# Kernel optimization log

Measured on AMD Instinct MI355X. Metric: run time of the kernel, lower is better.

## Reference

```python
import jax, jax.numpy as jnp
import numpy as np
from jax import lax

K = 21            # length_p_kernel
PK = K * K        # 441
CENTER = PK // 2  # 220, center of prediction window
EPS = 1e-4
PAD = K // 2


def conv3(x, w, b):
    # 3x3 same-padding conv, NCHW / OIHW
    y = lax.conv_general_dilated(x, w, (1, 1), ((1, 1), (1, 1)),
                                 dimension_numbers=('NCHW', 'OIHW', 'NCHW'))
    return y + b[None, :, None, None]


def unfold(x):
    # torch F.unfold with 21x21 kernel, zero padding 10 -> [b, C, 441, h, w]
    b, c, h, w = x.shape
    p = lax.conv_general_dilated_patches(x, (K, K), (1, 1), ((PAD, PAD), (PAD, PAD)))
    return p.reshape(b, c, PK, h, w)


def setup_inputs() -> dict:
    key = jax.random.key(0)
    ks = jax.random.split(key, 6)
    inp = jax.random.normal(ks[0], (1, 10, 128, 128), dtype=jnp.float32)
    ref = jax.random.normal(ks[1], (1, 3, 128, 128), dtype=jnp.float32)
    w0 = jax.random.normal(ks[2], (100, 10, 3, 3), dtype=jnp.float32) * 0.05
    b0 = jnp.zeros((100,), jnp.float32)
    wmid = jax.random.normal(ks[3], (23, 100, 100, 3, 3), dtype=jnp.float32) * 0.05
    bmid = jnp.zeros((23, 100), jnp.float32)
    wfin = jax.random.normal(ks[4], (441, 100, 3, 3), dtype=jnp.float32) * 0.05
    bfin = jnp.zeros((441,), jnp.float32)
    return {"input": inp, "ref": ref, "w0": w0, "b0": b0,
            "wmid": wmid, "bmid": bmid, "wfin": wfin, "bfin": bfin}


def reference(input, ref, w0, b0, wmid, bmid, wfin, bfin):
    # ref is only used by the (unavailable) loss branch; only_img_out path computed.
    b, _, h, w = input.shape

    x = conv3(input, w0, b0)

    def step(x, wb):
        return jax.nn.leaky_relu(conv3(x, wb[0], wb[1]), 0.01), None
    x, _ = lax.scan(step, x, (wmid, bmid))

    # --- W generator + softmax over 441 kernel-weight channels ---
    W = jax.nn.softmax(conv3(x, wfin, bfin), axis=1)        # [b,441,h,w]
    Wp = jnp.transpose(W, (0, 2, 3, 1))                      # [b,h,w,441]

    # --- design matrix: [1, aux features] unfolded into 21x21 windows ---
    ones = jnp.ones((b, 1, h, w), input.dtype)
    design = jnp.concatenate([ones, input[:, 3:]], axis=1)   # [b,8,h,w]
    XT = jnp.transpose(unfold(design), (0, 3, 4, 1, 2))      # [b,h,w,8,441]

    # --- weighted normal equations, per pixel ---
    XTW = XT * Wp[..., None, :]                              # [b,h,w,8,441]
    XTWX = jnp.einsum('bhwik,bhwjk->bhwij', XTW, XT)         # [b,h,w,8,8]
    reg = (jnp.eye(8, dtype=input.dtype) * EPS).at[0, 0].set(0.0)
    XTWX = XTWX + reg

    Y = jnp.transpose(unfold(input[:, :3]), (0, 3, 4, 2, 1)) # [b,h,w,441,3]
    XTWY = jnp.einsum('bhwik,bhwkc->bhwic', XTW, Y)          # [b,h,w,8,3]
    para = jnp.linalg.solve(XTWX, XTWY)                      # [b,h,w,8,3]

    # prediction at window center (loss_type == 0 path)
    domain = XT[..., CENTER]                                 # [b,h,w,8]
    out = jnp.einsum('bhwi,bhwic->bhwc', domain, para)       # [b,h,w,3]
    return jnp.transpose(out, (0, 3, 1, 2))                  # [b,3,h,w]
```

## Files before the change

kernel.cpp:

```cpp
#include <hip/hip_runtime.h>
#include <hip/hip_bf16.h>

#define HW 128
#define NPIX (HW * HW)
#define HB 130
#define HPIX (HB * HB)
#define ITW 148
#define EPS 1e-4f

typedef __attribute__((ext_vector_type(4))) float f32x4;
typedef __attribute__((ext_vector_type(2))) float f32x2;
typedef _Float16 f16;
typedef __attribute__((ext_vector_type(8))) _Float16 f16x8;
typedef __attribute__((ext_vector_type(4))) _Float16 f16x4;
typedef __attribute__((ext_vector_type(4))) int i32x4;

__device__ __forceinline__ void gload16(const f16* g, f16* l) {
  __builtin_amdgcn_global_load_lds(
      (const __attribute__((address_space(1))) unsigned int*)(const void*)g,
      (__attribute__((address_space(3))) unsigned int*)(void*)l, 16, 0, 0);
}

__device__ __forceinline__ f32x2 shflx2(f32x2 v, int m) {
  double d = __builtin_bit_cast(double, v);
  d = __shfl_xor(d, m);
  return __builtin_bit_cast(f32x2, d);
}

__global__ __launch_bounds__(256) void zero_buf(i32x4* __restrict__ p, int n) {
  int i = blockIdx.x * 256 + threadIdx.x;
  if (i < n) p[i] = i32x4{0, 0, 0, 0};
}

__global__ __launch_bounds__(256) void prep_input_k(
    const float* __restrict__ in, float* __restrict__ itp) {
  int idx = blockIdx.x * 256 + threadIdx.x;
  if (idx >= ITW * ITW) return;
  int py = idx / ITW, px = idx - py * ITW;
  float v[16];
#pragma unroll
  for (int i = 0; i < 16; i++) v[i] = 0.f;
  if (py >= 10 && py < 138 && px >= 10 && px < 138) {
    int p = (py - 10) * HW + (px - 10);
    v[0] = 1.f;
#pragma unroll
    for (int c = 0; c < 10; c++) v[1 + c] = in[c * NPIX + p];
  }
  float4* op = (float4*)(itp + idx * 16);
#pragma unroll
  for (int g = 0; g < 4; g++)
    op[g] = make_float4(v[g * 4], v[g * 4 + 1], v[g * 4 + 2], v[g * 4 + 3]);
}

__global__ __launch_bounds__(256) void pack_wmid_k(
    const float* __restrict__ wm, f16* __restrict__ wb) {
  int idx = blockIdx.x * 256 + threadIdx.x;
  int e = idx & 7;
  int l = (idx >> 3) & 63;
  int kc = (idx >> 9) & 3;
  int cf = (idx >> 11) & 7;
  int tL = idx >> 14;
  int L = tL / 9;
  int t = tL - L * 9;
  int co = cf * 16 + (l & 15);
  int ci = kc * 32 + (l >> 4) * 8 + e;
  float v = 0.f;
  if (co < 100 && ci < 100) v = wm[((L * 100 + co) * 100 + ci) * 9 + t];
  wb[idx] = (f16)v;
}

__global__ __launch_bounds__(256) void pack_wfin_k(
    const float* __restrict__ wf, f16* __restrict__ wb) {
  int idx = blockIdx.x * 256 + threadIdx.x;
  int e = idx & 7;
  int l = (idx >> 3) & 63;
  int kc = (idx >> 9) & 3;
  int cf = (idx >> 11) & 31;
  int t = idx >> 16;
  int co = cf * 16 + (l & 15);
  int ci = kc * 32 + (l >> 4) * 8 + e;
  float v = 0.f;
  if (co < 441 && ci < 100) v = wf[(co * 100 + ci) * 9 + t];
  wb[idx] = (f16)v;
}

__global__ __launch_bounds__(256) void conv0_k(
    const float* __restrict__ in, const float* __restrict__ w0,
    const float* __restrict__ b0, f16* __restrict__ act) {
  const int tx = threadIdx.x & 15, ty = threadIdx.x >> 4;
  const int x = blockIdx.x * 16 + tx, y = blockIdx.y * 16 + ty;
  const int co0 = blockIdx.z * 16;
  const int nco = max(0, min(16, 100 - co0));
  float acc[16];
#pragma unroll
  for (int i = 0; i < 16; i++) acc[i] = (i < nco) ? b0[co0 + i] : 0.f;
  for (int ci = 0; ci < 10; ci++) {
    const float* ip = in + ci * NPIX;
    float v[9];
#pragma unroll
    for (int t = 0; t < 9; t++) {
      int ny = y + t / 3 - 1, nx = x + t % 3 - 1;
      bool ok = ((unsigned)ny < (unsigned)HW) && ((unsigned)nx < (unsigned)HW);
      v[t] = ok ? ip[ny * HW + nx] : 0.f;
    }
    const float* wp = w0 + (co0 * 10 + ci) * 9;
#pragma unroll
    for (int i = 0; i < 16; i++) {
      if (i < nco) {
#pragma unroll
        for (int t = 0; t < 9; t++)
          acc[i] = fmaf(wp[i * 90 + t], v[t], acc[i]);
      }
    }
  }
  f16* op = act + ((y + 1) * HB + (x + 1)) * 128 + co0;
#pragma unroll
  for (int g = 0; g < 4; g++) {
    f16x4 sv;
#pragma unroll
    for (int j = 0; j < 4; j++) sv[j] = (f16)acc[g * 4 + j];
    *(f16x4*)(op + g * 4) = sv;
  }
}

template <int NCF, bool FINAL>
__global__ __launch_bounds__(256) void conv_mfma_k(
    const f16* __restrict__ act, const f16* __restrict__ wb,
    const float* __restrict__ bias, f16* __restrict__ out) {
  __shared__ f16 ldsB[3 * 34 * 128];
  __shared__ f16 ldsA[8 * 4 * 64 * 8];
  f16x8* ldsB8 = (f16x8*)ldsB;
  const f16x8* actF8 = (const f16x8*)act;

  const int tid = threadIdx.x;
  const int l = tid & 63;
  const int w = tid >> 6;
  const int lr = l & 15;
  const int lg = l >> 4;

  constexpr int NB = FINAL ? 2048 : 512;
  const int lid = blockIdx.x + (FINAL ? 512 * blockIdx.y : 0);
  const int l2 = (lid & 7) * (NB >> 3) + (lid >> 3);
  const int cfq = FINAL ? (l2 >> 9) : 0;
  const int rem = l2 & 511;
  const int y = rem >> 2;
  const int x0 = (rem & 3) * 32;
  const int cf0 = cfq * 8;
  const int wslot = w * 4096;

#pragma unroll
  for (int it = 0; it < 7; it++) {
    int cid = it * 256 + tid;
    if (cid < 1632) {
      int row = cid / 544;
      int rem2 = cid - row * 544;
      int lp = rem2 >> 4;
      int c = rem2 & 15;
      f16x8 v = actF8[((y + row) * HB + x0 + lp) * 16 + (c ^ (lp & 7))];
      ldsB8[(row * 34 + lp) * 16 + c] = v;
    }
  }

#pragma unroll
  for (int j = 0; j < 8; j++)
    gload16(wb + (long)(0 * NCF + cf0 + 2 * w) * 2048 + j * 512 + l * 8,
            &ldsA[wslot + j * 512]);

  asm volatile("s_waitcnt lgkmcnt(0)" ::: "memory");
  __builtin_amdgcn_s_barrier();

  f32x4 acc[2][2];
#pragma unroll
  for (int m = 0; m < 2; m++)
#pragma unroll
    for (int n = 0; n < 2; n++) acc[m][n] = f32x4{0.f, 0.f, 0.f, 0.f};

#pragma unroll
  for (int t = 0; t < 9; t++) {
    asm volatile("s_waitcnt vmcnt(0)" ::: "memory");
    __builtin_amdgcn_sched_barrier(0);
    f16x8 af[2][4];
#pragma unroll
    for (int m = 0; m < 2; m++)
#pragma unroll
      for (int kc = 0; kc < 4; kc++)
        af[m][kc] =
            *(const f16x8*)&ldsA[wslot + ((m * 4 + kc) * 64 + l) * 8];
    asm volatile("s_waitcnt lgkmcnt(0)" ::: "memory");
    __builtin_amdgcn_sched_barrier(0);
    if (t < 8) {
#pragma unroll
      for (int j = 0; j < 8; j++)
        gload16(wb + (long)((t + 1) * NCF + cf0 + 2 * w) * 2048 + j * 512 + l * 8,
                &ldsA[wslot + j * 512]);
    }
    const int dx = t - (t / 3) * 3, r = t / 3;
    __builtin_amdgcn_s_setprio(1);
#pragma unroll
    for (int kc = 0; kc < 4; kc++) {
      const int kq = kc * 4 + lg;
      f16x8 fb[2];
#pragma unroll
      for (int n = 0; n < 2; n++) {
        const int lp = lr + n * 16 + dx;
        fb[n] = ldsB8[(r * 34 + lp) * 16 + (kq ^ (lp & 7))];
      }
#pragma unroll
      for (int m = 0; m < 2; m++) {
        acc[m][0] = __builtin_amdgcn_mfma_f32_16x16x32_f16(af[m][kc], fb[0], acc[m][0], 0, 0, 0);
        acc[m][1] = __builtin_amdgcn_mfma_f32_16x16x32_f16(af[m][kc], fb[1], acc[m][1], 0, 0, 0);
      }
    }
    __builtin_amdgcn_s_setprio(0);
  }

#pragma unroll
  for (int m = 0; m < 2; m++) {
#pragma unroll
    for (int n = 0; n < 2; n++) {
      int co = (cf0 + 2 * w + m) * 16 + lg * 4;
      int px = x0 + n * 16 + lr;
      if (FINAL && co >= 448) continue;
      f16x4 sv;
#pragma unroll
      for (int j = 0; j < 4; j++) {
        float v;
        if (FINAL) {
          v = (co + j < 441) ? acc[m][n][j] + bias[co + j] : -60000.f;
        } else {
          float bv = (co + j < 100) ? bias[co + j] : 0.f;
          v = acc[m][n][j] + bv;
          v = v > 0.f ? v : 0.01f * v;
        }
        sv[j] = (f16)v;
      }
      f16* op = FINAL ? out + (y * HW + px) * 448 + co
                      : out + ((y + 1) * HB + (px + 1)) * 128 + co;
      *(f16x4*)op = sv;
    }
  }
}

__global__ __launch_bounds__(256) void wls_k(
    const float* __restrict__ itp, const f16* __restrict__ logits,
    float* __restrict__ out) {
  const int tid = threadIdx.x;
  const int part = tid & 15;
  const int p = blockIdx.x * 16 + (tid >> 4);
  const int x = p & (HW - 1), y = p >> 7;
  const int hpc = (y + 10) * ITW + (x + 10);

  constexpr int roff[8] = {0, 4, 8, 11, 14, 16, 18, 19};
  constexpr int rnp[8] = {4, 4, 3, 3, 2, 2, 1, 1};

  const f16* lp = logits + p * 448 + part;
  f16 lgv[28];
#pragma unroll
  for (int j = 0; j < 28; j++) lgv[j] = lp[j * 16];

  float m = -1e30f;
#pragma unroll
  for (int j = 0; j < 28; j++) m = fmaxf(m, (float)lgv[j]);
  m = fmaxf(m, __shfl_xor(m, 1));
  m = fmaxf(m, __shfl_xor(m, 2));
  m = fmaxf(m, __shfl_xor(m, 4));
  m = fmaxf(m, __shfl_xor(m, 8));

  f32x2 A2[20];
#pragma unroll
  for (int i = 0; i < 20; i++) A2[i] = f32x2{0.f, 0.f};
  f32x2 Bm2[12];
#pragma unroll
  for (int i = 0; i < 12; i++) Bm2[i] = f32x2{0.f, 0.f};
  float S = 0.f;

  int ky = 0, kx = part;
#pragma unroll
  for (int j = 0; j < 28; j++) {
    const int k = part + 16 * j;
    const float u = __expf((float)lgv[j] - m);
    S += u;
    if (k < 441) {
      const float4* q =
          (const float4*)(itp + (hpc + (ky - 10) * ITW + (kx - 10)) * 16);
      float4 f0 = q[0], f1 = q[1], f2 = q[2];
      f32x2 xv2[4] = {{f0.x, f1.x}, {f1.y, f1.z}, {f1.w, f2.x}, {f2.y, f2.z}};
      f32x2 ux2[4];
#pragma unroll
      for (int rp = 0; rp < 4; rp++) ux2[rp] = u * xv2[rp];
#pragma unroll
      for (int i = 0; i < 8; i++) {
        const float uxi = ux2[i >> 1][i & 1];
        const f32x2 sp = {uxi, uxi};
        const int b2 = (i & ~1) >> 1;
#pragma unroll
        for (int pj = 0; pj < 4; pj++) {
          if (pj < rnp[i]) A2[roff[i] + pj] = sp * xv2[b2 + pj] + A2[roff[i] + pj];
        }
      }
      const float yv[3] = {f0.y, f0.z, f0.w};
#pragma unroll
      for (int c = 0; c < 3; c++) {
        const f32x2 ys = {yv[c], yv[c]};
#pragma unroll
        for (int rp = 0; rp < 4; rp++)
          Bm2[c * 4 + rp] = ys * ux2[rp] + Bm2[c * 4 + rp];
      }
    }
    kx += 16;
    if (kx >= 21) { kx -= 21; ky += 1; }
  }

#pragma unroll
  for (int i = 0; i < 20; i++) {
    A2[i] += shflx2(A2[i], 1);
    A2[i] += shflx2(A2[i], 2);
    A2[i] += shflx2(A2[i], 4);
    A2[i] += shflx2(A2[i], 8);
  }
#pragma unroll
  for (int i = 0; i < 12; i++) {
    Bm2[i] += shflx2(Bm2[i], 1);
    Bm2[i] += shflx2(Bm2[i], 2);
    Bm2[i] += shflx2(Bm2[i], 4);
    Bm2[i] += shflx2(Bm2[i], 8);
  }
  S += __shfl_xor(S, 1);
  S += __shfl_xor(S, 2);
  S += __shfl_xor(S, 4);
  S += __shfl_xor(S, 8);

  float M[8][8], R[8][3];
#pragma unroll
  for (int i = 0; i < 8; i++) {
#pragma unroll
    for (int j = 0; j < 8; j++) {
      const int lo = (i < j) ? i : j;
      const int hi = (i < j) ? j : i;
      const int d = hi - (lo & ~1);
      M[i][j] = A2[roff[lo] + (d >> 1)][d & 1];
    }
#pragma unroll
    for (int c = 0; c < 3; c++) R[i][c] = Bm2[c * 4 + (i >> 1)][i & 1];
  }
#pragma unroll
  for (int i = 1; i < 8; i++) M[i][i] += S * EPS;

#pragma unroll
  for (int c = 0; c < 8; c++) {
    const float inv = 1.f / M[c][c];
#pragma unroll
    for (int r = c + 1; r < 8; r++) {
      const float f = M[r][c] * inv;
#pragma unroll
      for (int j = c + 1; j < 8; j++) M[r][j] = fmaf(-f, M[c][j], M[r][j]);
#pragma unroll
      for (int cc = 0; cc < 3; cc++) R[r][cc] = fmaf(-f, R[c][cc], R[r][cc]);
    }
  }
  float para[8][3];
#pragma unroll
  for (int r = 7; r >= 0; r--) {
#pragma unroll
    for (int cc = 0; cc < 3; cc++) {
      float s = R[r][cc];
#pragma unroll
      for (int j = r + 1; j < 8; j++) s = fmaf(-M[r][j], para[j][cc], s);
      para[r][cc] = s / M[r][r];
    }
  }

  const float4* qc = (const float4*)(itp + hpc * 16);
  float4 c1 = qc[1], c2 = qc[2];
  float dv[8] = {1.f, c1.x, c1.y, c1.z, c1.w, c2.x, c2.y, c2.z};
  if (part < 3) {
    float res = 0.f;
#pragma unroll
    for (int i = 0; i < 8; i++) res = fmaf(dv[i], para[i][part], res);
    out[part * NPIX + p] = res;
  }
}

extern "C" void kernel_launch(void* const* d_in, const int* in_sizes, int n_in,
                              void* d_out, int out_size, void* d_ws, size_t ws_size,
                              hipStream_t stream) {
  const float* input = (const float*)d_in[0];
  const float* w0 = (const float*)d_in[2];
  const float* b0 = (const float*)d_in[3];
  const float* wmid = (const float*)d_in[4];
  const float* bmid = (const float*)d_in[5];
  const float* wfin = (const float*)d_in[6];
  const float* bfin = (const float*)d_in[7];
  float* out = (float*)d_out;

  f16* act0 = (f16*)d_ws;
  f16* act1 = act0 + HPIX * 128;
  f16* logits = act1 + HPIX * 128;
  f16* wbuf = logits + NPIX * 448;
  f16* wfbuf = wbuf + 23 * 9 * 16384;
  float* inputT = (float*)(wfbuf + 9 * 65536);

  {
    int n = (2 * HPIX * 128 * 2) / 16;
    zero_buf<<<(n + 255) / 256, 256, 0, stream>>>((i32x4*)act0, n);
  }
  prep_input_k<<<(ITW * ITW + 255) / 256, 256, 0, stream>>>(input, inputT);
  pack_wmid_k<<<(23 * 9 * 16384) / 256, 256, 0, stream>>>(wmid, wbuf);
  pack_wfin_k<<<(9 * 65536) / 256, 256, 0, stream>>>(wfin, wfbuf);

  conv0_k<<<dim3(8, 8, 8), 256, 0, stream>>>(input, w0, b0, act0);

  for (int L = 0; L < 23; L++) {
    const f16* src = (L & 1) ? act1 : act0;
    f16* dst = (L & 1) ? act0 : act1;
    conv_mfma_k<8, false><<<dim3(512, 1), 256, 0, stream>>>(
        src, wbuf + (long)L * 9 * 16384, bmid + L * 100, dst);
  }
  conv_mfma_k<32, true><<<dim3(512, 4), 256, 0, stream>>>(
      act1, wfbuf, bfin, logits);

  wls_k<<<NPIX * 16 / 256, 256, 0, stream>>>(inputT, logits, out);
}
```

Before: 355.5 us.

## Tile conv blocks over two output rows to reuse weight fragments

```diff
diff --git a/kernel.cpp b/kernel.cpp
--- a/kernel.cpp
+++ b/kernel.cpp
@@ -123,11 +123,17 @@
   }
 }
 
-template <int NCF, bool FINAL>
+template <int NCF, int PX, bool FINAL>
 __global__ __launch_bounds__(256) void conv_mfma_k(
     const f16* __restrict__ act, const f16* __restrict__ wb,
     const float* __restrict__ bias, f16* __restrict__ out) {
-  __shared__ f16 ldsB[3 * 34 * 128];
+  constexpr int PY = 2;
+  constexpr int XB = HW / PX;
+  constexpr int LPW = PX + 2;
+  constexpr int NN = PX / 16;
+  constexpr int GEOM = (HW / PY) * XB;
+  constexpr int NB = FINAL ? GEOM * 4 : GEOM;
+  __shared__ f16 ldsB[(PY + 2) * LPW * 128];
   __shared__ f16 ldsA[8 * 4 * 64 * 8];
   f16x8* ldsB8 = (f16x8*)ldsB;
   const f16x8* actF8 = (const f16x8*)act;
@@ -138,26 +144,26 @@
   const int lr = l & 15;
   const int lg = l >> 4;
 
-  constexpr int NB = FINAL ? 2048 : 512;
-  const int lid = blockIdx.x + (FINAL ? 512 * blockIdx.y : 0);
+  const int lid = blockIdx.x;
   const int l2 = (lid & 7) * (NB >> 3) + (lid >> 3);
-  const int cfq = FINAL ? (l2 >> 9) : 0;
-  const int rem = l2 & 511;
-  const int y = rem >> 2;
-  const int x0 = (rem & 3) * 32;
+  const int cfq = FINAL ? (l2 / GEOM) : 0;
+  const int rem = l2 % GEOM;
+  const int y0 = (rem / XB) * PY;
+  const int x0 = (rem % XB) * PX;
   const int cf0 = cfq * 8;
   const int wslot = w * 4096;
 
-#pragma unroll
-  for (int it = 0; it < 7; it++) {
+  constexpr int NCH = (PY + 2) * LPW * 16;
+#pragma unroll
+  for (int it = 0; it < (NCH + 255) / 256; it++) {
     int cid = it * 256 + tid;
-    if (cid < 1632) {
-      int row = cid / 544;
-      int rem2 = cid - row * 544;
+    if (cid < NCH) {
+      int row = cid / (LPW * 16);
+      int rem2 = cid - row * (LPW * 16);
       int lp = rem2 >> 4;
       int c = rem2 & 15;
-      f16x8 v = actF8[((y + row) * HB + x0 + lp) * 16 + (c ^ (lp & 7))];
-      ldsB8[(row * 34 + lp) * 16 + c] = v;
+      f16x8 v = actF8[((y0 + row) * HB + x0 + lp) * 16 + (c ^ (lp & 7))];
+      ldsB8[(row * LPW + lp) * 16 + c] = v;
     }
   }
 
@@ -169,11 +175,13 @@
   asm volatile("s_waitcnt lgkmcnt(0)" ::: "memory");
   __builtin_amdgcn_s_barrier();
 
-  f32x4 acc[2][2];
+  f32x4 acc[2][NN][PY];
 #pragma unroll
   for (int m = 0; m < 2; m++)
 #pragma unroll
-    for (int n = 0; n < 2; n++) acc[m][n] = f32x4{0.f, 0.f, 0.f, 0.f};
+    for (int n = 0; n < NN; n++)
+#pragma unroll
+      for (int rr = 0; rr < PY; rr++) acc[m][n][rr] = f32x4{0.f, 0.f, 0.f, 0.f};
 
 #pragma unroll
   for (int t = 0; t < 9; t++) {
@@ -199,44 +207,53 @@
 #pragma unroll
     for (int kc = 0; kc < 4; kc++) {
       const int kq = kc * 4 + lg;
-      f16x8 fb[2];
-#pragma unroll
-      for (int n = 0; n < 2; n++) {
-        const int lp = lr + n * 16 + dx;
-        fb[n] = ldsB8[(r * 34 + lp) * 16 + (kq ^ (lp & 7))];
+      f16x8 fb[NN][PY];
+#pragma unroll
+      for (int n = 0; n < NN; n++)
+#pragma unroll
+        for (int rr = 0; rr < PY; rr++) {
+          const int lp = lr + n * 16 + dx;
+          fb[n][rr] = ldsB8[((r + rr) * LPW + lp) * 16 + (kq ^ (lp & 7))];
+        }
+#pragma unroll
+      for (int m = 0; m < 2; m++)
+#pragma unroll
+        for (int n = 0; n < NN; n++)
+#pragma unroll
+          for (int rr = 0; rr < PY; rr++)
+            acc[m][n][rr] = __builtin_amdgcn_mfma_f32_16x16x32_f16(
+                af[m][kc], fb[n][rr], acc[m][n][rr], 0, 0, 0);
+    }
+    __builtin_amdgcn_s_setprio(0);
+  }
+
+#pragma unroll
+  for (int m = 0; m < 2; m++) {
+#pragma unroll
+    for (int n = 0; n < NN; n++) {
+#pragma unroll
+      for (int rr = 0; rr < PY; rr++) {
+        int co = (cf0 + 2 * w + m) * 16 + lg * 4;
+        int px = x0 + n * 16 + lr;
+        int yy = y0 + rr;
+        if (FINAL && co >= 448) continue;
+        f16x4 sv;
+#pragma unroll
+        for (int j = 0; j < 4; j++) {
+          float v;
+          if (FINAL) {
+            v = (co + j < 441) ? acc[m][n][rr][j] + bias[co + j] : -60000.f;
+          } else {
+            float bv = (co + j < 100) ? bias[co + j] : 0.f;
+            v = acc[m][n][rr][j] + bv;
+            v = v > 0.f ? v : 0.01f * v;
+          }
+          sv[j] = (f16)v;
+        }
+        f16* op = FINAL ? out + (yy * HW + px) * 448 + co
+                        : out + ((yy + 1) * HB + (px + 1)) * 128 + co;
+        *(f16x4*)op = sv;
       }
-#pragma unroll
-      for (int m = 0; m < 2; m++) {
-        acc[m][0] = __builtin_amdgcn_mfma_f32_16x16x32_f16(af[m][kc], fb[0], acc[m][0], 0, 0, 0);
-        acc[m][1] = __builtin_amdgcn_mfma_f32_16x16x32_f16(af[m][kc], fb[1], acc[m][1], 0, 0, 0);
-      }
-    }
-    __builtin_amdgcn_s_setprio(0);
-  }
-
-#pragma unroll
-  for (int m = 0; m < 2; m++) {
-#pragma unroll
-    for (int n = 0; n < 2; n++) {
-      int co = (cf0 + 2 * w + m) * 16 + lg * 4;
-      int px = x0 + n * 16 + lr;
-      if (FINAL && co >= 448) continue;
-      f16x4 sv;
-#pragma unroll
-      for (int j = 0; j < 4; j++) {
-        float v;
-        if (FINAL) {
-          v = (co + j < 441) ? acc[m][n][j] + bias[co + j] : -60000.f;
-        } else {
-          float bv = (co + j < 100) ? bias[co + j] : 0.f;
-          v = acc[m][n][j] + bv;
-          v = v > 0.f ? v : 0.01f * v;
-        }
-        sv[j] = (f16)v;
-      }
-      f16* op = FINAL ? out + (y * HW + px) * 448 + co
-                      : out + ((y + 1) * HB + (px + 1)) * 128 + co;
-      *(f16x4*)op = sv;
     }
   }
 }
@@ -413,10 +430,10 @@
   for (int L = 0; L < 23; L++) {
     const f16* src = (L & 1) ? act1 : act0;
     f16* dst = (L & 1) ? act0 : act1;
-    conv_mfma_k<8, false><<<dim3(512, 1), 256, 0, stream>>>(
+    conv_mfma_k<8, 16, false><<<dim3(512), 256, 0, stream>>>(
         src, wbuf + (long)L * 9 * 16384, bmid + L * 100, dst);
   }
-  conv_mfma_k<32, true><<<dim3(512, 4), 256, 0, stream>>>(
+  conv_mfma_k<32, 32, true><<<dim3(1024), 256, 0, stream>>>(
       act1, wfbuf, bfin, logits);
 
   wls_k<<<NPIX * 16 / 256, 256, 0, stream>>>(inputT, logits, out);
```

Result: faster. 342.5 us (-3.6%).
